# Kernel optimization log

Hardware: AMD Instinct MI355X
Metric: run time of the kernel (lower is better)

Reference implementation:

```python
import jax, jax.numpy as jnp
import numpy as np

B, L, D, K = 32, 512, 512, 3
LOG_2PI = float(np.log(2.0 * np.pi))


def conv1d(x, w, b):
    # x: (B, L, 1), w: (D, 1, K), b: (D,) -> (B, L, D); padding = (K-1)//2
    pad = (w.shape[-1] - 1) // 2
    y = jax.lax.conv_general_dilated(
        x.transpose(0, 2, 1), w, window_strides=(1,), padding=[(pad, pad)],
        dimension_numbers=('NCH', 'OIH', 'NCH'))
    return y.transpose(0, 2, 1) + b


def setup_inputs() -> dict:
    ks = jax.random.split(jax.random.key(0), 14)
    x = jax.random.normal(ks[0], (B, L, D), dtype=jnp.float32)
    durations_float = jax.random.uniform(ks[1], (B, L), dtype=jnp.float32) * 8.0
    durations_int = jax.random.randint(ks[2], (B, L), 1, 8, dtype=jnp.int32)
    energies = jax.random.normal(ks[3], (B, L), dtype=jnp.float32)
    pitch = jax.random.normal(ks[4], (B, L), dtype=jnp.float32)
    input_lengths = jax.random.randint(ks[5], (B,), L // 2, L + 1, dtype=jnp.int32)
    input_lengths = input_lengths.at[0].set(L)  # ensure max length == L (torch masks at max(lengths))
    s = 0.05
    w_dur = jax.random.normal(ks[6], (D, 1, K), dtype=jnp.float32) * s
    b_dur = jax.random.normal(ks[7], (D,), dtype=jnp.float32) * s
    w_en = jax.random.normal(ks[8], (D, 1, K), dtype=jnp.float32) * s
    b_en = jax.random.normal(ks[9], (D,), dtype=jnp.float32) * s
    w_pitch = jax.random.normal(ks[10], (D, 1, K), dtype=jnp.float32) * s
    b_pitch = jax.random.normal(ks[11], (D,), dtype=jnp.float32) * s
    w_lin = jax.random.normal(ks[12], (1, D), dtype=jnp.float32) * s
    b_lin = jax.random.normal(ks[13], (1,), dtype=jnp.float32) * s
    nb_frames = int(jnp.max(jnp.cumsum(durations_int, axis=1)))  # concrete static T
    return dict(x=x, durations_float=durations_float, durations_int=durations_int,
                energies=energies, pitch=pitch, input_lengths=input_lengths,
                w_dur=w_dur, b_dur=b_dur, w_en=w_en, b_en=b_en,
                w_pitch=w_pitch, b_pitch=b_pitch, w_lin=w_lin, b_lin=b_lin,
                nb_frames=nb_frames)


def reference(x, durations_float, durations_int, energies, pitch, input_lengths,
              w_dur, b_dur, w_en, b_en, w_pitch, b_pitch, w_lin, b_lin, nb_frames):
    Bb, Ll, Dd = x.shape
    dur_e = conv1d(durations_float[..., None], w_dur, b_dur)   # (B, L, D)
    en_e = conv1d(energies[..., None], w_en, b_en)
    pi_e = conv1d(pitch[..., None], w_pitch, b_pitch)
    x = x + en_e + pi_e
    range_inputs = x + dur_e
    ranges = jax.nn.softplus(range_inputs @ w_lin.T + b_lin)[..., 0]  # (B, L)
    valid = jnp.arange(Ll) < input_lengths[:, None]                   # (B, L) True = valid
    ranges = jnp.where(valid, ranges, 1.0)
    d = durations_int.astype(x.dtype)
    cumsum = jnp.cumsum(durations_int, axis=1)
    means = d * 0.5 + jnp.concatenate(
        [jnp.zeros((Bb, 1), x.dtype), cumsum[:, :-1].astype(x.dtype)], axis=1)  # (B, L)
    frames = jnp.arange(nb_frames, dtype=x.dtype) + 0.5                # (T,)
    z = (frames[None, None, :] - means[..., None]) / ranges[..., None] # (B, L, T)
    log_probs = -0.5 * z * z - jnp.log(ranges)[..., None] - 0.5 * LOG_2PI
    probs = jnp.where(valid[..., None], jnp.exp(log_probs), 0.0)       # (B, L, T)
    weights = probs / (jnp.sum(probs, axis=1, keepdims=True) + 1e-20)
    # torch: sum_L x[b,l,d] * w[b,l,t] -> (B, D, T), then permute -> (B, T, D)
    x_upsamp = jnp.einsum('bld,blt->btd', x, weights)
    return x_upsamp, weights
```

## Files before the change

### kernel.cpp

```cpp
#include <hip/hip_runtime.h>
#include <hip/hip_bf16.h>
#include <stdint.h>

#define NB 32
#define NL 512
#define ND 512

typedef __bf16 bf16x8 __attribute__((ext_vector_type(8)));
typedef float  f32x4  __attribute__((ext_vector_type(4)));

__device__ __forceinline__ unsigned short f2bf(float f) {
    uint32_t u = __float_as_uint(f);
    u = (u + 0x7fffu + ((u >> 16) & 1u)) >> 16;
    return (unsigned short)u;
}


__global__ __launch_bounds__(256) void fuse2_kernel(
    const float* __restrict__ x, const float* __restrict__ df,
    const float* __restrict__ en, const float* __restrict__ pi,
    const int* __restrict__ lens,
    const float* __restrict__ w_dur, const float* __restrict__ b_dur,
    const float* __restrict__ w_en,  const float* __restrict__ b_en,
    const float* __restrict__ w_pi,  const float* __restrict__ b_pi,
    const float* __restrict__ w_lin, const float* __restrict__ b_lin,
    unsigned short* __restrict__ Xb, float* __restrict__ ranges)
{
    const int blk = blockIdx.x;
    const int b   = blk >> 6;
    const int lb  = (blk & 63) << 3;
    const int tid = threadIdx.x;
    const int d0  = tid << 1;

    float we[2][3], wp[2][3], wd[2][3], bev[2], bpv[2], bdv[2], wl[2];
    #pragma unroll
    for (int q = 0; q < 2; ++q) {
        const int d = d0 + q;
        #pragma unroll
        for (int k = 0; k < 3; ++k) {
            we[q][k] = w_en[d*3+k];
            wp[q][k] = w_pi[d*3+k];
            wd[q][k] = w_dur[d*3+k];
        }
        bev[q] = b_en[d]; bpv[q] = b_pi[d]; bdv[q] = b_dur[d]; wl[q] = w_lin[d];
    }

    float acc[8];
    #pragma unroll
    for (int i = 0; i < 8; ++i) acc[i] = 0.f;

    uint4 chunk[2];
    unsigned short* cu = (unsigned short*)chunk;

    #pragma unroll
    for (int li = 0; li < 8; ++li) {
        const int l  = lb + li;
        const int bl = (b << 9) + l;
        const float dm1 = (l > 0)      ? df[bl-1] : 0.f;
        const float dc  = df[bl];
        const float dp1 = (l < NL-1)   ? df[bl+1] : 0.f;
        const float em1 = (l > 0)      ? en[bl-1] : 0.f;
        const float ec  = en[bl];
        const float ep1 = (l < NL-1)   ? en[bl+1] : 0.f;
        const float pm1 = (l > 0)      ? pi[bl-1] : 0.f;
        const float pc  = pi[bl];
        const float pp1 = (l < NL-1)   ? pi[bl+1] : 0.f;
        const float2 xv = *(const float2*)&x[(size_t)bl * ND + d0];
        #pragma unroll
        for (int q = 0; q < 2; ++q) {
            const float ev  = we[q][0]*em1 + we[q][1]*ec + we[q][2]*ep1 + bev[q];
            const float pv  = wp[q][0]*pm1 + wp[q][1]*pc + wp[q][2]*pp1 + bpv[q];
            const float xxv = (q ? xv.y : xv.x) + ev + pv;
            cu[q*8 + li] = f2bf(xxv);
            const float dv  = wd[q][0]*dm1 + wd[q][1]*dc + wd[q][2]*dp1 + bdv[q];
            acc[li] += (xxv + dv) * wl[q];
        }
    }
    #pragma unroll
    for (int q = 0; q < 2; ++q) {
        const int d = d0 + q;
        const size_t off = (size_t)b * (NL * ND)
            + (size_t)(((lb >> 5) << 5) + (d >> 4)) * 512
            + (size_t)((((lb >> 3) & 3) << 4) + (d & 15)) * 8;
        *(uint4*)&Xb[off] = chunk[q];
    }

    #pragma unroll
    for (int li = 0; li < 8; ++li)
        #pragma unroll
        for (int off = 32; off; off >>= 1)
            acc[li] += __shfl_down(acc[li], off, 64);
    __shared__ float red[4][8];
    const int lane = tid & 63, wid = tid >> 6;
    if (lane == 0)
        #pragma unroll
        for (int li = 0; li < 8; ++li) red[wid][li] = acc[li];
    __syncthreads();
    if (tid < 8) {
        const float s = red[0][tid] + red[1][tid] + red[2][tid] + red[3][tid] + b_lin[0];
        float r = fmaxf(s, 0.f) + log1pf(expf(-fabsf(s)));
        if (lb + tid >= lens[b]) r = 1.0f;
        ranges[(b << 9) + lb + tid] = r;
    }
}


#define STAGE_X2(kk, buf) do {                                                  \
    const char* src_ = Bbase + (size_t)(kk) * 32768;                            \
    char* dst_ = smem + (buf) * 32768;                                          \
    _Pragma("unroll")                                                           \
    for (int c = 0; c < 4; ++c) {                                               \
        const int o_ = (wid * 4 + c) * 1024;                                    \
        __builtin_amdgcn_global_load_lds(                                       \
            (__attribute__((address_space(1))) void*)(src_ + o_ + lane * 16),   \
            (__attribute__((address_space(3))) void*)(dst_ + o_), 16, 0, 0);    \
    }                                                                           \
} while (0)

#define GENP2(kk, buf) do {                                                     \
    const int l0_ = (kk) * 32 + oct * 4;                                        \
    float pv_[4];                                                               \
    unsigned short pu_[4];                                                      \
    _Pragma("unroll")                                                           \
    for (int j = 0; j < 4; ++j) {                                               \
        const float zz = fmaf(ftv, t_sinv[l0_ + j], t_nms[l0_ + j]);            \
        pv_[j] = t_sc[l0_ + j] * __expf(-0.5f * zz * zz);                       \
        pu_[j] = f2bf(pv_[j]);                                                  \
    }                                                                           \
    char* pd_ = smem + 65536 + (buf) * 4096 + (tloc >> 4) * 1024               \
              + (((oct >> 1) << 4) + (tloc & 15)) * 16 + ((oct & 1) << 3);      \
    *(uint2*)pd_ = *(uint2*)pu_;                                                \
    if (tvalid) {                                                               \
        _Pragma("unroll")                                                       \
        for (int j = 0; j < 4; ++j)                                             \
            wout[((size_t)(b << 9) + l0_ + j) * T + tglb] = pv_[j] * myDinv;    \
    }                                                                           \
} while (0)

__global__ __launch_bounds__(512, 4) void fusedwg2_kernel(
    const unsigned short* __restrict__ Xb,
    const float* __restrict__ ranges, const int* __restrict__ di,
    const int* __restrict__ lens,
    float* __restrict__ wout, float* __restrict__ xup, int T)
{
    __shared__ __align__(16) char smem[80128];
    float* t_sinv = (float*)(smem + 73728);
    float* t_nms  = (float*)(smem + 75776);
    float* t_sc   = (float*)(smem + 77824);
    float* dinvL  = (float*)(smem + 79872);
    int*   scanA  = (int*)smem;
    int*   scanB  = (int*)(smem + 2048);
    float* partial = (float*)(smem + 4096);

    const int tid  = threadIdx.x;
    const int lane = tid & 63, wid = tid >> 6;
    const int wn   = wid;

    const int i    = blockIdx.x;
    const int xcd  = i & 7, slot = i >> 3;
    const int b    = (xcd << 2) + (slot & 3);
    const int m    = slot >> 2;
    const int m64  = m << 6;

    const int tloc = tid & 63;
    const int oct  = tid >> 6;
    const int tglb = m64 + tloc;
    const bool tvalid = tglb < T;
    const float ftv = (float)tglb + 0.5f;

    const int dv = di[(b << 9) + tid];
    scanA[tid] = dv;
    __syncthreads();
    {
        int* src = scanA; int* dst = scanB;
        #pragma unroll
        for (int off = 1; off < NL; off <<= 1) {
            dst[tid] = src[tid] + (tid >= off ? src[tid - off] : 0);
            __syncthreads();
            int* tmp = src; src = dst; dst = tmp;
        }
        const float mu = (float)src[tid] - 0.5f * (float)dv;
        const float r  = ranges[(b << 9) + tid];
        const float inv = 1.f / r;
        t_sinv[tid] = inv;
        t_nms[tid]  = -mu * inv;
        t_sc[tid]   = (tid < lens[b]) ? 0.3989422804014327f * inv : 0.f;
    }
    __syncthreads();

    {
        float s = 0.f;
        const int lbeg = oct << 6;
        #pragma unroll 4
        for (int l = lbeg; l < lbeg + 64; ++l) {
            const float zz = fmaf(ftv, t_sinv[l], t_nms[l]);
            s += t_sc[l] * __expf(-0.5f * zz * zz);
        }
        partial[(oct << 6) + tloc] = s;
    }
    __syncthreads();
    if (tid < 64) {
        float sum = 0.f;
        #pragma unroll
        for (int o = 0; o < 8; ++o) sum += partial[(o << 6) + tid];
        dinvL[tid] = 1.f / (sum + 1e-20f);
    }
    __syncthreads();
    const float myDinv = dinvL[tloc];

    const char* Bbase = (const char*)Xb + (size_t)b * (NL * ND * 2);

    f32x4 acc[4][4];
    #pragma unroll
    for (int ii = 0; ii < 4; ++ii)
        #pragma unroll
        for (int jj = 0; jj < 4; ++jj) acc[ii][jj] = (f32x4){0.f, 0.f, 0.f, 0.f};

    STAGE_X2(0, 0);
    __builtin_amdgcn_sched_barrier(0);
    GENP2(0, 0);

    for (int k = 0; k < 16; ++k) {
        asm volatile("s_waitcnt vmcnt(4) lgkmcnt(0)" ::: "memory");
        __builtin_amdgcn_s_barrier();
        __builtin_amdgcn_sched_barrier(0);
        const int cur = k & 1;
        if (k < 15) {
            STAGE_X2(k + 1, cur ^ 1);
            __builtin_amdgcn_sched_barrier(0);
            GENP2(k + 1, cur ^ 1);
        }
        bf16x8 af[4], bfr[4];
        #pragma unroll
        for (int ii = 0; ii < 4; ++ii)
            af[ii] = *(const bf16x8*)(smem + 65536 + cur * 4096 + ii * 1024 + lane * 16);
        #pragma unroll
        for (int jj = 0; jj < 4; ++jj)
            bfr[jj] = *(const bf16x8*)(smem + cur * 32768 + ((wn << 2) + jj) * 1024 + lane * 16);
        #pragma unroll
        for (int ii = 0; ii < 4; ++ii)
            #pragma unroll
            for (int jj = 0; jj < 4; ++jj)
                acc[ii][jj] = __builtin_amdgcn_mfma_f32_16x16x32_bf16(af[ii], bfr[jj], acc[ii][jj], 0, 0, 0);
    }

    float* lf = (float*)smem;
    float* Ob = xup + (size_t)b * T * ND;
    #pragma unroll
    for (int c = 0; c < 4; ++c) {
        __syncthreads();
        #pragma unroll
        for (int jj = 0; jj < 4; ++jj)
            #pragma unroll
            for (int r = 0; r < 4; ++r) {
                const int row = ((lane >> 4) << 2) + r;
                const int col = (wn << 6) + (jj << 4) + (lane & 15);
                lf[row * 516 + col] = acc[c][jj][r];
            }
        __syncthreads();
        const int trow = tid >> 7;
        const int colq = (tid & 127) << 2;
        #pragma unroll
        for (int s = 0; s < 4; ++s) {
            const int row = trow + (s << 2);
            const int t = m64 + (c << 4) + row;
            if (t < T) {
                const float dsc = dinvL[(c << 4) + row];
                f32x4 v = *(const f32x4*)(lf + row * 516 + colq);
                v[0] *= dsc; v[1] *= dsc; v[2] *= dsc; v[3] *= dsc;
                *(f32x4*)&Ob[(size_t)t * ND + colq] = v;
            }
        }
    }
}

__global__ __launch_bounds__(512) void means_kernel(
    const int* __restrict__ di, float* __restrict__ means)
{
    const int b = blockIdx.x;
    const int l = threadIdx.x;
    __shared__ int s[NL];
    const int d = di[b * NL + l];
    s[l] = d;
    __syncthreads();
    #pragma unroll
    for (int off = 1; off < NL; off <<= 1) {
        const int v = (l >= off) ? s[l - off] : 0;
        __syncthreads();
        s[l] += v;
        __syncthreads();
    }
    means[b * NL + l] = 0.5f * (float)d + (float)(s[l] - d);
}

__global__ __launch_bounds__(256) void fuse_kernel(
    const float* __restrict__ x, const float* __restrict__ df,
    const float* __restrict__ en, const float* __restrict__ pi,
    const int* __restrict__ lens,
    const float* __restrict__ w_dur, const float* __restrict__ b_dur,
    const float* __restrict__ w_en,  const float* __restrict__ b_en,
    const float* __restrict__ w_pi,  const float* __restrict__ b_pi,
    const float* __restrict__ w_lin, const float* __restrict__ b_lin,
    float* __restrict__ xx, float* __restrict__ ranges)
{
    const int bl = blockIdx.x;
    const int b  = bl >> 9;
    const int l  = bl & (NL - 1);
    const int tid = threadIdx.x;
    const float dm1 = (l > 0)      ? df[bl - 1] : 0.f;
    const float d0  = df[bl];
    const float dp1 = (l < NL - 1) ? df[bl + 1] : 0.f;
    const float em1 = (l > 0)      ? en[bl - 1] : 0.f;
    const float e0  = en[bl];
    const float ep1 = (l < NL - 1) ? en[bl + 1] : 0.f;
    const float pm1 = (l > 0)      ? pi[bl - 1] : 0.f;
    const float p0  = pi[bl];
    const float pp1 = (l < NL - 1) ? pi[bl + 1] : 0.f;
    float acc = 0.f;
    #pragma unroll
    for (int d = tid; d < ND; d += 256) {
        const float xv = x[(size_t)bl * ND + d];
        const float ev = w_en[d*3]*em1 + w_en[d*3+1]*e0 + w_en[d*3+2]*ep1 + b_en[d];
        const float pv = w_pi[d*3]*pm1 + w_pi[d*3+1]*p0 + w_pi[d*3+2]*pp1 + b_pi[d];
        const float xxv = xv + ev + pv;
        xx[(size_t)bl * ND + d] = xxv;
        const float dv = w_dur[d*3]*dm1 + w_dur[d*3+1]*d0 + w_dur[d*3+2]*dp1 + b_dur[d];
        acc += (xxv + dv) * w_lin[d];
    }
    #pragma unroll
    for (int off = 32; off; off >>= 1) acc += __shfl_down(acc, off, 64);
    __shared__ float red[4];
    const int lane = tid & 63, wid = tid >> 6;
    if (lane == 0) red[wid] = acc;
    __syncthreads();
    if (tid == 0) {
        const float s = red[0] + red[1] + red[2] + red[3] + b_lin[0];
        float r = fmaxf(s, 0.f) + log1pf(expf(-fabsf(s)));
        if (l >= lens[b]) r = 1.0f;
        ranges[bl] = r;
    }
}

__global__ __launch_bounds__(256) void weights_kernel(
    const float* __restrict__ ranges, const float* __restrict__ means,
    const int* __restrict__ lens, float* __restrict__ weights, int T)
{
    const int b = blockIdx.y;
    const int t = blockIdx.x * 256 + threadIdx.x;
    __shared__ float sm[NL], sinv[NL], sc[NL];
    const int len = lens[b];
    for (int l = threadIdx.x; l < NL; l += 256) {
        const float r = ranges[b * NL + l];
        const float inv = 1.f / r;
        sm[l] = means[b * NL + l];
        sinv[l] = inv;
        sc[l] = (l < len) ? 0.3989422804014327f * inv : 0.f;
    }
    __syncthreads();
    if (t >= T) return;
    const float ft = (float)t + 0.5f;
    float sum = 0.f;
    #pragma unroll 4
    for (int l = 0; l < NL; ++l) {
        const float z = (ft - sm[l]) * sinv[l];
        sum += sc[l] * __expf(-0.5f * z * z);
    }
    const float dinv = 1.f / (sum + 1e-20f);
    #pragma unroll 4
    for (int l = 0; l < NL; ++l) {
        const float z = (ft - sm[l]) * sinv[l];
        weights[((size_t)b * NL + l) * T + t] = sc[l] * __expf(-0.5f * z * z) * dinv;
    }
}

#define BM 64
#define BN 64
#define BK 16
__global__ __launch_bounds__(256) void gemm_f32_kernel(
    const float* __restrict__ xx, const float* __restrict__ weights,
    float* __restrict__ out, int T)
{
    const int b  = blockIdx.z;
    const int t0 = blockIdx.y * BM;
    const int d0 = blockIdx.x * BN;
    const float* __restrict__ W = weights + (size_t)b * NL * T;
    const float* __restrict__ X = xx + (size_t)b * NL * ND;
    float* __restrict__ O = out + (size_t)b * T * ND;
    __shared__ float As[BK][BM];
    __shared__ float Bs[BK][BN];
    const int tid = threadIdx.x;
    const int tx = tid & 15;
    const int ty = tid >> 4;
    const int lr = tid >> 4;
    const int lc = (tid & 15) * 4;
    const bool vec_ok = (t0 + BM <= T) && ((T & 3) == 0);
    float acc[4][4] = {};
    for (int l0 = 0; l0 < NL; l0 += BK) {
        if (vec_ok) {
            *(float4*)&As[lr][lc] = *(const float4*)&W[(size_t)(l0 + lr) * T + t0 + lc];
        } else {
            #pragma unroll
            for (int j = 0; j < 4; ++j) {
                const int tcol = t0 + lc + j;
                As[lr][lc + j] = (tcol < T) ? W[(size_t)(l0 + lr) * T + tcol] : 0.f;
            }
        }
        *(float4*)&Bs[lr][lc] = *(const float4*)&X[(size_t)(l0 + lr) * ND + d0 + lc];
        __syncthreads();
        #pragma unroll
        for (int k = 0; k < BK; ++k) {
            float a[4], bb[4];
            *(float4*)a  = *(const float4*)&As[k][ty * 4];
            *(float4*)bb = *(const float4*)&Bs[k][tx * 4];
            #pragma unroll
            for (int i = 0; i < 4; ++i)
                #pragma unroll
                for (int j = 0; j < 4; ++j)
                    acc[i][j] += a[i] * bb[j];
        }
        __syncthreads();
    }
    #pragma unroll
    for (int i = 0; i < 4; ++i) {
        const int t = t0 + ty * 4 + i;
        if (t < T)
            *(float4*)&O[(size_t)t * ND + d0 + tx * 4] =
                make_float4(acc[i][0], acc[i][1], acc[i][2], acc[i][3]);
    }
}

extern "C" void kernel_launch(void* const* d_in, const int* in_sizes, int n_in,
                              void* d_out, int out_size, void* d_ws, size_t ws_size,
                              hipStream_t stream) {
    const float* x     = (const float*)d_in[0];
    const float* df    = (const float*)d_in[1];
    const int*   di    = (const int*)  d_in[2];
    const float* en    = (const float*)d_in[3];
    const float* pi    = (const float*)d_in[4];
    const int*   lens  = (const int*)  d_in[5];
    const float* w_dur = (const float*)d_in[6];
    const float* b_dur = (const float*)d_in[7];
    const float* w_en  = (const float*)d_in[8];
    const float* b_en  = (const float*)d_in[9];
    const float* w_pi  = (const float*)d_in[10];
    const float* b_pi  = (const float*)d_in[11];
    const float* w_lin = (const float*)d_in[12];
    const float* b_lin = (const float*)d_in[13];

    const int B = NB, L = NL, D = ND;
    const int T = out_size / (B * (L + D));
    const int MT = (T + 63) / 64;

    float* xup  = (float*)d_out;
    float* wout = xup + (size_t)B * T * D;

    const size_t XbBytes = (size_t)B * L * D * 2;
    const size_t need = XbBytes + (size_t)B * L * sizeof(float);

    if (ws_size >= need) {
        unsigned short* Xb = (unsigned short*)d_ws;
        float* ranges = (float*)(Xb + (size_t)B * L * D);

        hipLaunchKernelGGL(fuse2_kernel, dim3(B * 64), dim3(256), 0, stream,
                           x, df, en, pi, lens, w_dur, b_dur, w_en, b_en,
                           w_pi, b_pi, w_lin, b_lin, Xb, ranges);
        hipLaunchKernelGGL(fusedwg2_kernel, dim3(MT * 32), dim3(512), 0, stream,
                           Xb, ranges, di, lens, wout, xup, T);
    } else {
        float* xx     = (float*)d_ws;
        float* ranges = xx + (size_t)B * L * D;
        float* means  = ranges + (size_t)B * L;
        hipLaunchKernelGGL(fuse_kernel, dim3(B * L), dim3(256), 0, stream,
                           x, df, en, pi, lens, w_dur, b_dur, w_en, b_en,
                           w_pi, b_pi, w_lin, b_lin, xx, ranges);
        hipLaunchKernelGGL(means_kernel, dim3(B), dim3(512), 0, stream, di, means);
        hipLaunchKernelGGL(weights_kernel, dim3((T + 255) / 256, B), dim3(256), 0, stream,
                           ranges, means, lens, wout, T);
        hipLaunchKernelGGL(gemm_f32_kernel, dim3(D / BN, (T + BM - 1) / BM, B), dim3(256), 0, stream,
                           xx, wout, xup, T);
    }
}
```

Baseline: 101.5 us.

## Overlap first X stage with scan, defer weight stores past MFMA, use exp2

The first bf16 X tile load now starts before the duration scan; to make that safe, the scan scratch moves to LDS offsets that do not overlap the staging buffer. The Gaussian is rewritten so the constants fold into exp2f. Weight output stores are split from probability generation and issued after the MFMA block, raising wave priority during the matrix ops. Both outputs use nontemporal stores. The changes aim to hide global-load and store latency behind compute, at the cost of keeping probabilities live in registers across the MFMA section.

```diff
diff --git a/kernel.cpp b/kernel.cpp
--- a/kernel.cpp
+++ b/kernel.cpp
@@ -105,6 +105,8 @@
 }
 
 
+#define C2F 0.84932180028801904272f
+
 #define STAGE_X2(kk, buf) do {                                                  \
     const char* src_ = Bbase + (size_t)(kk) * 32768;                            \
     char* dst_ = smem + (buf) * 32768;                                          \
@@ -117,40 +119,44 @@
     }                                                                           \
 } while (0)
 
-#define GENP2(kk, buf) do {                                                     \
+#define GENP_COMP(kk, buf) do {                                                 \
     const int l0_ = (kk) * 32 + oct * 4;                                        \
-    float pv_[4];                                                               \
     unsigned short pu_[4];                                                      \
     _Pragma("unroll")                                                           \
     for (int j = 0; j < 4; ++j) {                                               \
-        const float zz = fmaf(ftv, t_sinv[l0_ + j], t_nms[l0_ + j]);            \
-        pv_[j] = t_sc[l0_ + j] * __expf(-0.5f * zz * zz);                       \
-        pu_[j] = f2bf(pv_[j]);                                                  \
+        const float u_ = fmaf(ftv, t_a[l0_ + j], t_b[l0_ + j]);                 \
+        pvv[j] = t_sc[l0_ + j] * exp2f(-u_ * u_);                               \
+        pu_[j] = f2bf(pvv[j]);                                                  \
     }                                                                           \
-    char* pd_ = smem + 65536 + (buf) * 4096 + (tloc >> 4) * 1024               \
+    char* pd_ = smem + 65536 + (buf) * 4096 + (tloc >> 4) * 1024                \
               + (((oct >> 1) << 4) + (tloc & 15)) * 16 + ((oct & 1) << 3);      \
     *(uint2*)pd_ = *(uint2*)pu_;                                                \
+} while (0)
+
+#define GENP_STORE(kk) do {                                                     \
+    const int l0_ = (kk) * 32 + oct * 4;                                        \
     if (tvalid) {                                                               \
         _Pragma("unroll")                                                       \
         for (int j = 0; j < 4; ++j)                                             \
-            wout[((size_t)(b << 9) + l0_ + j) * T + tglb] = pv_[j] * myDinv;    \
+            __builtin_nontemporal_store(pvv[j] * myDinv,                        \
+                woutb + (size_t)(l0_ + j) * T);                                 \
     }                                                                           \
 } while (0)
 
-__global__ __launch_bounds__(512, 4) void fusedwg2_kernel(
+__global__ __launch_bounds__(512, 4) void fusedwg3_kernel(
     const unsigned short* __restrict__ Xb,
     const float* __restrict__ ranges, const int* __restrict__ di,
     const int* __restrict__ lens,
     float* __restrict__ wout, float* __restrict__ xup, int T)
 {
     __shared__ __align__(16) char smem[80128];
-    float* t_sinv = (float*)(smem + 73728);
-    float* t_nms  = (float*)(smem + 75776);
-    float* t_sc   = (float*)(smem + 77824);
-    float* dinvL  = (float*)(smem + 79872);
-    int*   scanA  = (int*)smem;
-    int*   scanB  = (int*)(smem + 2048);
-    float* partial = (float*)(smem + 4096);
+    float* t_a   = (float*)(smem + 73728);
+    float* t_b   = (float*)(smem + 75776);
+    float* t_sc  = (float*)(smem + 77824);
+    float* dinvL = (float*)(smem + 79872);
+    int*   scanA = (int*)(smem + 65536);
+    int*   scanB = (int*)(smem + 67584);
+    float* partial = (float*)(smem + 69632);
 
     const int tid  = threadIdx.x;
     const int lane = tid & 63, wid = tid >> 6;
@@ -168,6 +174,10 @@
     const bool tvalid = tglb < T;
     const float ftv = (float)tglb + 0.5f;
 
+    const char* Bbase = (const char*)Xb + (size_t)b * (NL * ND * 2);
+
+    STAGE_X2(0, 0);
+
     const int dv = di[(b << 9) + tid];
     scanA[tid] = dv;
     __syncthreads();
@@ -182,9 +192,9 @@
         const float mu = (float)src[tid] - 0.5f * (float)dv;
         const float r  = ranges[(b << 9) + tid];
         const float inv = 1.f / r;
-        t_sinv[tid] = inv;
-        t_nms[tid]  = -mu * inv;
-        t_sc[tid]   = (tid < lens[b]) ? 0.3989422804014327f * inv : 0.f;
+        t_a[tid]  = inv * C2F;
+        t_b[tid]  = -mu * inv * C2F;
+        t_sc[tid] = (tid < lens[b]) ? 0.3989422804014327f * inv : 0.f;
     }
     __syncthreads();
 
@@ -193,8 +203,8 @@
         const int lbeg = oct << 6;
         #pragma unroll 4
         for (int l = lbeg; l < lbeg + 64; ++l) {
-            const float zz = fmaf(ftv, t_sinv[l], t_nms[l]);
-            s += t_sc[l] * __expf(-0.5f * zz * zz);
+            const float u = fmaf(ftv, t_a[l], t_b[l]);
+            s += t_sc[l] * exp2f(-u * u);
         }
         partial[(oct << 6) + tloc] = s;
     }
@@ -207,8 +217,7 @@
     }
     __syncthreads();
     const float myDinv = dinvL[tloc];
-
-    const char* Bbase = (const char*)Xb + (size_t)b * (NL * ND * 2);
+    float* woutb = wout + (size_t)(b << 9) * T + tglb;
 
     f32x4 acc[4][4];
     #pragma unroll
@@ -216,9 +225,9 @@
         #pragma unroll
         for (int jj = 0; jj < 4; ++jj) acc[ii][jj] = (f32x4){0.f, 0.f, 0.f, 0.f};
 
-    STAGE_X2(0, 0);
-    __builtin_amdgcn_sched_barrier(0);
-    GENP2(0, 0);
+    float pvv[4];
+    GENP_COMP(0, 0);
+    GENP_STORE(0);
 
     for (int k = 0; k < 16; ++k) {
         asm volatile("s_waitcnt vmcnt(4) lgkmcnt(0)" ::: "memory");
@@ -228,7 +237,7 @@
         if (k < 15) {
             STAGE_X2(k + 1, cur ^ 1);
             __builtin_amdgcn_sched_barrier(0);
-            GENP2(k + 1, cur ^ 1);
+            GENP_COMP(k + 1, cur ^ 1);
         }
         bf16x8 af[4], bfr[4];
         #pragma unroll
@@ -237,11 +246,15 @@
         #pragma unroll
         for (int jj = 0; jj < 4; ++jj)
             bfr[jj] = *(const bf16x8*)(smem + cur * 32768 + ((wn << 2) + jj) * 1024 + lane * 16);
+        __builtin_amdgcn_s_setprio(1);
         #pragma unroll
         for (int ii = 0; ii < 4; ++ii)
             #pragma unroll
             for (int jj = 0; jj < 4; ++jj)
                 acc[ii][jj] = __builtin_amdgcn_mfma_f32_16x16x32_bf16(af[ii], bfr[jj], acc[ii][jj], 0, 0, 0);
+        __builtin_amdgcn_s_setprio(0);
+        __builtin_amdgcn_sched_barrier(0);
+        if (k < 15) GENP_STORE(k + 1);
     }
 
     float* lf = (float*)smem;
@@ -268,7 +281,7 @@
                 const float dsc = dinvL[(c << 4) + row];
                 f32x4 v = *(const f32x4*)(lf + row * 516 + colq);
                 v[0] *= dsc; v[1] *= dsc; v[2] *= dsc; v[3] *= dsc;
-                *(f32x4*)&Ob[(size_t)t * ND + colq] = v;
+                __builtin_nontemporal_store(v, (f32x4*)&Ob[(size_t)t * ND + colq]);
             }
         }
     }
@@ -464,7 +477,7 @@
         hipLaunchKernelGGL(fuse2_kernel, dim3(B * 64), dim3(256), 0, stream,
                            x, df, en, pi, lens, w_dur, b_dur, w_en, b_en,
                            w_pi, b_pi, w_lin, b_lin, Xb, ranges);
-        hipLaunchKernelGGL(fusedwg2_kernel, dim3(MT * 32), dim3(512), 0, stream,
+        hipLaunchKernelGGL(fusedwg3_kernel, dim3(MT * 32), dim3(512), 0, stream,
                            Xb, ranges, di, lens, wout, xup, T);
     } else {
         float* xx     = (float*)d_ws;
```

Measured after the change: 118.7 us. 1.17x slower.
